# Performance work log

Hardware: AMD Instinct MI355X
Metric: run time of the kernel (lower is better)

## Reference

```python
import jax, jax.numpy as jnp
import numpy as np

N_NODES = 50000
N_EDGES = 600000
D_IN = 128
D_H = 128


def _sage_layer(h, src, dst, deg_inv, W_self, W_neigh, b):
    # gather src features along edges, sum into dst, then mean-normalize
    msum = jax.ops.segment_sum(h[src], dst, num_segments=N_NODES)  # [N, d]
    h_neigh = msum * deg_inv[:, None]
    return h @ W_self + h_neigh @ W_neigh + b


def setup_inputs() -> dict:
    key = jax.random.key(0)
    ks = jax.random.split(key, 10)
    inp = {
        'g_features': jax.random.normal(ks[0], (N_NODES, D_IN), dtype=jnp.float32),
        'src': jax.random.randint(ks[1], (N_EDGES,), 0, N_NODES, dtype=jnp.int32),
        'dst': jax.random.randint(ks[2], (N_EDGES,), 0, N_NODES, dtype=jnp.int32),
    }
    scale_in = 1.0 / np.sqrt(D_IN)
    scale_h = 1.0 / np.sqrt(D_H)
    inp['W_self1'] = jax.random.normal(ks[3], (D_IN, D_H), dtype=jnp.float32) * scale_in
    inp['W_neigh1'] = jax.random.normal(ks[4], (D_IN, D_H), dtype=jnp.float32) * scale_in
    inp['b1'] = jnp.zeros((D_H,), dtype=jnp.float32)
    inp['W_self2'] = jax.random.normal(ks[5], (D_H, D_H), dtype=jnp.float32) * scale_h
    inp['W_neigh2'] = jax.random.normal(ks[6], (D_H, D_H), dtype=jnp.float32) * scale_h
    inp['b2'] = jnp.zeros((D_H,), dtype=jnp.float32)
    inp['W_self3'] = jax.random.normal(ks[7], (D_H, D_H), dtype=jnp.float32) * scale_h
    inp['W_neigh3'] = jax.random.normal(ks[8], (D_H, D_H), dtype=jnp.float32) * scale_h
    inp['b3'] = jnp.zeros((D_H,), dtype=jnp.float32)
    return inp


def reference(g_features, src, dst, W_self1, W_neigh1, b1, W_self2, W_neigh2, b2, W_self3, W_neigh3, b3):
    # in-degree per dst node, clamped to >= 1 (DGL SAGEConv mean)
    deg = jax.ops.segment_sum(jnp.ones_like(dst, dtype=g_features.dtype), dst, num_segments=N_NODES)
    deg_inv = 1.0 / jnp.maximum(deg, 1.0)

    h = _sage_layer(g_features, src, dst, deg_inv, W_self1, W_neigh1, b1)
    h = jax.nn.relu(h)
    h = _sage_layer(h, src, dst, deg_inv, W_self2, W_neigh2, b2)
    h = jax.nn.relu(h)
    h = _sage_layer(h, src, dst, deg_inv, W_self3, W_neigh3, b3)
    return h
```

## Files before the change

kernel.cpp:

```cpp
#include <hip/hip_runtime.h>
#include <hip/hip_bf16.h>

#define N_NODES 50000
#define N_EDGES 600000
#define D 128

typedef __bf16 bf16x8 __attribute__((ext_vector_type(8)));
typedef float f32x4 __attribute__((ext_vector_type(4)));

__device__ __forceinline__ float bits2f(unsigned int u) {
    union { unsigned int i; float f; } t; t.i = u; return t.f;
}
__device__ __forceinline__ unsigned short f2bf(float x) {
    unsigned int u = __builtin_bit_cast(unsigned int, x);
    unsigned int r = (u + 0x7fff + ((u >> 16) & 1)) >> 16;
    return (unsigned short)r;
}

__global__ void hist_kernel(const int* __restrict__ dst, int* __restrict__ deg, int n) {
    int i = blockIdx.x * blockDim.x + threadIdx.x;
    if (i < n) atomicAdd(&deg[dst[i]], 1);
}

__global__ void scan1_kernel(const int* __restrict__ deg, int* __restrict__ partial,
                             int* __restrict__ blk_sums) {
    __shared__ int ws[16];
    int i = blockIdx.x * 1024 + threadIdx.x;
    int x = (i < N_NODES) ? deg[i] : 0;
    int lane = threadIdx.x & 63, wid = threadIdx.x >> 6;
    int v = x;
    #pragma unroll
    for (int off = 1; off < 64; off <<= 1) {
        int t = __shfl_up(v, off);
        if (lane >= off) v += t;
    }
    if (lane == 63) ws[wid] = v;
    __syncthreads();
    if (threadIdx.x == 0) {
        int c = 0;
        #pragma unroll
        for (int j = 0; j < 16; ++j) { int t = ws[j]; ws[j] = c; c += t; }
        blk_sums[blockIdx.x] = c;
    }
    __syncthreads();
    if (i < N_NODES) partial[i] = v - x + ws[wid];
}

__global__ void scan2_kernel(int* __restrict__ blk_sums, int nb) {
    int lane = threadIdx.x;
    int v = (lane < nb) ? blk_sums[lane] : 0;
    int x = v;
    #pragma unroll
    for (int off = 1; off < 64; off <<= 1) {
        int t = __shfl_up(v, off);
        if (lane >= off) v += t;
    }
    if (lane < nb) blk_sums[lane] = v - x;
}

__global__ void scan3_kernel(const int* __restrict__ partial, const int* __restrict__ blk_sums,
                             const int* __restrict__ deg, int* __restrict__ row_start,
                             int* __restrict__ cursor, float* __restrict__ deg_inv) {
    int i = blockIdx.x * 256 + threadIdx.x;
    if (i < N_NODES) {
        int rs = partial[i] + blk_sums[i >> 10];
        row_start[i] = rs;
        cursor[i] = rs;
        deg_inv[i] = 1.0f / fmaxf((float)deg[i], 1.0f);
    }
    if (i == 0) row_start[N_NODES] = N_EDGES;
}

__global__ void fill_kernel(const int* __restrict__ src, const int* __restrict__ dst,
                            int* __restrict__ cursor, int* __restrict__ esrc, int n) {
    int i = blockIdx.x * blockDim.x + threadIdx.x;
    if (i < n) {
        int p = atomicAdd(&cursor[dst[i]], 1);
        esrc[p] = src[i];
    }
}

__global__ void cvt_feat_kernel(const float* __restrict__ in, unsigned short* __restrict__ out, int n4) {
    int i = blockIdx.x * blockDim.x + threadIdx.x;
    if (i < n4) {
        float4 v = *(const float4*)(in + (size_t)i * 4);
        ushort4 o;
        o.x = f2bf(v.x); o.y = f2bf(v.y); o.z = f2bf(v.z); o.w = f2bf(v.w);
        *(ushort4*)(out + (size_t)i * 4) = o;
    }
}

__global__ void cvt_w_kernel(const float* w0, const float* w1, const float* w2,
                             const float* w3, const float* w4, const float* w5,
                             unsigned short* __restrict__ o) {
    int m = blockIdx.x >> 6;
    int j = (blockIdx.x & 63) * 256 + threadIdx.x;
    const float* src = m == 0 ? w0 : m == 1 ? w1 : m == 2 ? w2 : m == 3 ? w3 : m == 4 ? w4 : w5;
    int n = j >> 7, k = j & 127;
    o[m * 16384 + n * 128 + k] = f2bf(src[k * 128 + n]);
}

__device__ __forceinline__ void acc_add(float* a, uint4 v) {
    unsigned int w[4] = {v.x, v.y, v.z, v.w};
    #pragma unroll
    for (int j = 0; j < 4; ++j) {
        a[2*j]   += bits2f(w[j] << 16);
        a[2*j+1] += bits2f(w[j] & 0xffff0000u);
    }
}

#define AGG_TPB 256
__global__ __launch_bounds__(AGG_TPB) void agg_kernel(
        const unsigned short* __restrict__ h, const int* __restrict__ row_start,
        const int* __restrict__ esrc, const float* __restrict__ deg_inv,
        unsigned short* __restrict__ msum) {
    int node = blockIdx.x * (AGG_TPB / 16) + (threadIdx.x >> 4);
    if (node >= N_NODES) return;
    int l = threadIdx.x & 15;
    int s = row_start[node], e = row_start[node + 1];
    const unsigned short* hl = h + l * 8;
    float acc[8] = {0, 0, 0, 0, 0, 0, 0, 0};
    int k = s;
    for (; k + 4 <= e; k += 4) {
        int i0 = esrc[k], i1 = esrc[k + 1], i2 = esrc[k + 2], i3 = esrc[k + 3];
        uint4 v0 = *(const uint4*)(hl + (size_t)i0 * D);
        uint4 v1 = *(const uint4*)(hl + (size_t)i1 * D);
        uint4 v2 = *(const uint4*)(hl + (size_t)i2 * D);
        uint4 v3 = *(const uint4*)(hl + (size_t)i3 * D);
        acc_add(acc, v0); acc_add(acc, v1); acc_add(acc, v2); acc_add(acc, v3);
    }
    for (; k < e; ++k) {
        uint4 v = *(const uint4*)(hl + (size_t)esrc[k] * D);
        acc_add(acc, v);
    }
    float di = deg_inv[node];
    unsigned short o[8];
    #pragma unroll
    for (int j = 0; j < 8; ++j) o[j] = f2bf(acc[j] * di);
    *(uint4*)(msum + (size_t)node * D + l * 8) = *(uint4*)o;
}

__global__ __launch_bounds__(256) void gemm_kernel(
        const unsigned short* __restrict__ h, const unsigned short* __restrict__ msum,
        const unsigned short* __restrict__ WsT, const unsigned short* __restrict__ WnT,
        const float* __restrict__ bias, void* __restrict__ outp,
        int do_relu, int store_f32) {
    __shared__ char lds[49152];
    char* As = lds;
    char* Bs = lds + 16384;
    int tid = threadIdx.x;
    int l = tid & 63;
    int w = tid >> 6;
    int row0 = blockIdx.x * 64;

    f32x4 acc[4][2];
    #pragma unroll
    for (int mt = 0; mt < 4; ++mt)
        #pragma unroll
        for (int nt = 0; nt < 2; ++nt)
            acc[mt][nt] = (f32x4)0.0f;

    for (int phase = 0; phase < 2; ++phase) {
        const unsigned short* A = phase ? msum : h;
        const unsigned short* B = phase ? WnT : WsT;
        if (phase) __syncthreads();
        #pragma unroll
        for (int i = 0; i < 4; ++i) {
            int c = tid + i * 256;
            int r = c >> 4, kb = (c & 15) << 4;
            int gr = row0 + r; if (gr >= N_NODES) gr = N_NODES - 1;
            uint4 v = *(const uint4*)(A + (size_t)gr * D + ((c & 15) << 3));
            *(uint4*)(As + r * 256 + (kb ^ ((r & 7) << 4))) = v;
        }
        #pragma unroll
        for (int i = 0; i < 8; ++i) {
            int c = tid + i * 256;
            int r = c >> 4, kb = (c & 15) << 4;
            uint4 v = *(const uint4*)(B + (size_t)r * D + ((c & 15) << 3));
            *(uint4*)(Bs + r * 256 + (kb ^ ((r & 7) << 4))) = v;
        }
        __syncthreads();

        #pragma unroll
        for (int ks = 0; ks < 4; ++ks) {
            int kb = ks * 64 + ((l >> 4) << 4);
            bf16x8 a[4], b[2];
            #pragma unroll
            for (int mt = 0; mt < 4; ++mt) {
                int r = mt * 16 + (l & 15);
                a[mt] = *(const bf16x8*)(As + r * 256 + (kb ^ ((r & 7) << 4)));
            }
            #pragma unroll
            for (int nt = 0; nt < 2; ++nt) {
                int r = w * 32 + nt * 16 + (l & 15);
                b[nt] = *(const bf16x8*)(Bs + r * 256 + (kb ^ ((r & 7) << 4)));
            }
            #pragma unroll
            for (int mt = 0; mt < 4; ++mt)
                #pragma unroll
                for (int nt = 0; nt < 2; ++nt)
                    acc[mt][nt] = __builtin_amdgcn_mfma_f32_16x16x32_bf16(a[mt], b[nt], acc[mt][nt], 0, 0, 0);
        }
    }

    #pragma unroll
    for (int nt = 0; nt < 2; ++nt) {
        int col = w * 32 + nt * 16 + (l & 15);
        float bv = bias[col];
        #pragma unroll
        for (int mt = 0; mt < 4; ++mt) {
            #pragma unroll
            for (int r = 0; r < 4; ++r) {
                int grow = row0 + mt * 16 + ((l >> 4) << 2) + r;
                if (grow < N_NODES) {
                    float v = acc[mt][nt][r] + bv;
                    if (do_relu) v = fmaxf(v, 0.f);
                    if (store_f32) ((float*)outp)[(size_t)grow * D + col] = v;
                    else ((unsigned short*)outp)[(size_t)grow * D + col] = f2bf(v);
                }
            }
        }
    }
}

static inline size_t align_up(size_t x, size_t a) { return (x + a - 1) & ~(a - 1); }

extern "C" void kernel_launch(void* const* d_in, const int* in_sizes, int n_in,
                              void* d_out, int out_size, void* d_ws, size_t ws_size,
                              hipStream_t stream) {
    const float* g_feat = (const float*)d_in[0];
    const int* src = (const int*)d_in[1];
    const int* dst = (const int*)d_in[2];
    const float* Ws1 = (const float*)d_in[3];
    const float* Wn1 = (const float*)d_in[4];
    const float* b1  = (const float*)d_in[5];
    const float* Ws2 = (const float*)d_in[6];
    const float* Wn2 = (const float*)d_in[7];
    const float* b2  = (const float*)d_in[8];
    const float* Ws3 = (const float*)d_in[9];
    const float* Wn3 = (const float*)d_in[10];
    const float* b3  = (const float*)d_in[11];
    float* out = (float*)d_out;

    char* ws = (char*)d_ws;
    int* deg        = (int*)ws;            ws += align_up(N_NODES * 4, 256);
    int* row_start  = (int*)ws;            ws += align_up((N_NODES + 1) * 4, 256);
    int* cursor     = (int*)ws;            ws += align_up(N_NODES * 4, 256);
    float* deg_inv  = (float*)ws;          ws += align_up(N_NODES * 4, 256);
    int* partial    = (int*)ws;            ws += align_up(N_NODES * 4, 256);
    int* blk_sums   = (int*)ws;            ws += align_up(64 * 4, 256);
    int* esrc       = (int*)ws;            ws += align_up(N_EDGES * 4, 256);
    unsigned short* g_bf = (unsigned short*)ws;  ws += align_up((size_t)N_NODES * D * 2, 256);
    unsigned short* WT   = (unsigned short*)ws;  ws += align_up(6 * 128 * 128 * 2, 256);
    unsigned short* bufA = (unsigned short*)ws;  ws += align_up((size_t)N_NODES * D * 2, 256);
    unsigned short* bufB = (unsigned short*)ws;  ws += align_up((size_t)N_NODES * D * 2, 256);
    unsigned short* bufM = (unsigned short*)ws;  ws += align_up((size_t)N_NODES * D * 2, 256);

    hipMemsetAsync(deg, 0, N_NODES * 4, stream);
    hist_kernel<<<(N_EDGES + 255) / 256, 256, 0, stream>>>(dst, deg, N_EDGES);
    cvt_feat_kernel<<<((N_NODES * D / 4) + 255) / 256, 256, 0, stream>>>(g_feat, g_bf, N_NODES * D / 4);
    cvt_w_kernel<<<6 * 64, 256, 0, stream>>>(Ws1, Wn1, Ws2, Wn2, Ws3, Wn3, WT);
    int nb = (N_NODES + 1023) / 1024;
    scan1_kernel<<<nb, 1024, 0, stream>>>(deg, partial, blk_sums);
    scan2_kernel<<<1, 64, 0, stream>>>(blk_sums, nb);
    scan3_kernel<<<(N_NODES + 255) / 256, 256, 0, stream>>>(partial, blk_sums, deg, row_start, cursor, deg_inv);
    fill_kernel<<<(N_EDGES + 255) / 256, 256, 0, stream>>>(src, dst, cursor, esrc, N_EDGES);

    dim3 agg_grid((N_NODES * 16 + AGG_TPB - 1) / AGG_TPB);
    dim3 gemm_grid((N_NODES + 63) / 64);
    const unsigned short *WsT1 = WT, *WnT1 = WT + 16384, *WsT2 = WT + 2*16384,
                         *WnT2 = WT + 3*16384, *WsT3 = WT + 4*16384, *WnT3 = WT + 5*16384;

    agg_kernel<<<agg_grid, AGG_TPB, 0, stream>>>(g_bf, row_start, esrc, deg_inv, bufM);
    gemm_kernel<<<gemm_grid, 256, 0, stream>>>(g_bf, bufM, WsT1, WnT1, b1, bufA, 1, 0);
    agg_kernel<<<agg_grid, AGG_TPB, 0, stream>>>(bufA, row_start, esrc, deg_inv, bufM);
    gemm_kernel<<<gemm_grid, 256, 0, stream>>>(bufA, bufM, WsT2, WnT2, b2, bufB, 1, 0);
    agg_kernel<<<agg_grid, AGG_TPB, 0, stream>>>(bufB, row_start, esrc, deg_inv, bufM);
    gemm_kernel<<<gemm_grid, 256, 0, stream>>>(bufB, bufM, WsT3, WnT3, b3, out, 0, 1);
}
```

Baseline: 292.2 us.

## Fuse neighbor aggregation into layer GEMM and merge prep kernels

Fuses each layer's mean-aggregation into the GEMM kernel: every block aggregates 32 nodes directly into LDS and then runs the self and neighbor matmuls, with weight fragments held in registers. This removes the msum buffer write and read plus three launches. The feature conversion, degree histogram and weight transpose are also merged into one prep kernel to cut launch overhead. The trade-off is smaller GEMM tiles with more register pressure, and a gather-heavy phase that stalls before the MFMA phase within each block.

Result: slower. 320.6 us (+9.7%).

```diff
diff --git a/kernel.cpp b/kernel.cpp
--- a/kernel.cpp
+++ b/kernel.cpp
@@ -4,6 +4,7 @@
 #define N_NODES 50000
 #define N_EDGES 600000
 #define D 128
+#define BM 32
 
 typedef __bf16 bf16x8 __attribute__((ext_vector_type(8)));
 typedef float f32x4 __attribute__((ext_vector_type(4)));
@@ -17,9 +18,34 @@
     return (unsigned short)r;
 }
 
-__global__ void hist_kernel(const int* __restrict__ dst, int* __restrict__ deg, int n) {
-    int i = blockIdx.x * blockDim.x + threadIdx.x;
-    if (i < n) atomicAdd(&deg[dst[i]], 1);
+#define PREP_CVT_BLOCKS 6250
+#define PREP_HIST_BLOCKS 2344
+#define PREP_W_BLOCKS 384
+__global__ void prep_kernel(const float* __restrict__ feat, unsigned short* __restrict__ g_bf,
+                            const int* __restrict__ dst, int* __restrict__ deg,
+                            const float* w0, const float* w1, const float* w2,
+                            const float* w3, const float* w4, const float* w5,
+                            unsigned short* __restrict__ WT) {
+    int b = blockIdx.x;
+    if (b < PREP_CVT_BLOCKS) {
+        int i = b * 256 + threadIdx.x;
+        if (i < N_NODES * D / 4) {
+            float4 v = *(const float4*)(feat + (size_t)i * 4);
+            ushort4 o;
+            o.x = f2bf(v.x); o.y = f2bf(v.y); o.z = f2bf(v.z); o.w = f2bf(v.w);
+            *(ushort4*)(g_bf + (size_t)i * 4) = o;
+        }
+    } else if (b < PREP_CVT_BLOCKS + PREP_HIST_BLOCKS) {
+        int i = (b - PREP_CVT_BLOCKS) * 256 + threadIdx.x;
+        if (i < N_EDGES) atomicAdd(&deg[dst[i]], 1);
+    } else {
+        int j = (b - PREP_CVT_BLOCKS - PREP_HIST_BLOCKS) * 256 + threadIdx.x;
+        int m = j >> 14;
+        int e = j & 16383;
+        const float* src = m == 0 ? w0 : m == 1 ? w1 : m == 2 ? w2 : m == 3 ? w3 : m == 4 ? w4 : w5;
+        int n = e >> 7, k = e & 127;
+        WT[m * 16384 + n * 128 + k] = f2bf(src[k * 128 + n]);
+    }
 }
 
 __global__ void scan1_kernel(const int* __restrict__ deg, int* __restrict__ partial,
@@ -80,26 +106,6 @@
     }
 }
 
-__global__ void cvt_feat_kernel(const float* __restrict__ in, unsigned short* __restrict__ out, int n4) {
-    int i = blockIdx.x * blockDim.x + threadIdx.x;
-    if (i < n4) {
-        float4 v = *(const float4*)(in + (size_t)i * 4);
-        ushort4 o;
-        o.x = f2bf(v.x); o.y = f2bf(v.y); o.z = f2bf(v.z); o.w = f2bf(v.w);
-        *(ushort4*)(out + (size_t)i * 4) = o;
-    }
-}
-
-__global__ void cvt_w_kernel(const float* w0, const float* w1, const float* w2,
-                             const float* w3, const float* w4, const float* w5,
-                             unsigned short* __restrict__ o) {
-    int m = blockIdx.x >> 6;
-    int j = (blockIdx.x & 63) * 256 + threadIdx.x;
-    const float* src = m == 0 ? w0 : m == 1 ? w1 : m == 2 ? w2 : m == 3 ? w3 : m == 4 ? w4 : w5;
-    int n = j >> 7, k = j & 127;
-    o[m * 16384 + n * 128 + k] = f2bf(src[k * 128 + n]);
-}
-
 __device__ __forceinline__ void acc_add(float* a, uint4 v) {
     unsigned int w[4] = {v.x, v.y, v.z, v.w};
     #pragma unroll
@@ -109,97 +115,100 @@
     }
 }
 
-#define AGG_TPB 256
-__global__ __launch_bounds__(AGG_TPB) void agg_kernel(
+__global__ __launch_bounds__(256) void layer_kernel(
         const unsigned short* __restrict__ h, const int* __restrict__ row_start,
         const int* __restrict__ esrc, const float* __restrict__ deg_inv,
-        unsigned short* __restrict__ msum) {
-    int node = blockIdx.x * (AGG_TPB / 16) + (threadIdx.x >> 4);
-    if (node >= N_NODES) return;
-    int l = threadIdx.x & 15;
-    int s = row_start[node], e = row_start[node + 1];
-    const unsigned short* hl = h + l * 8;
-    float acc[8] = {0, 0, 0, 0, 0, 0, 0, 0};
-    int k = s;
-    for (; k + 4 <= e; k += 4) {
-        int i0 = esrc[k], i1 = esrc[k + 1], i2 = esrc[k + 2], i3 = esrc[k + 3];
-        uint4 v0 = *(const uint4*)(hl + (size_t)i0 * D);
-        uint4 v1 = *(const uint4*)(hl + (size_t)i1 * D);
-        uint4 v2 = *(const uint4*)(hl + (size_t)i2 * D);
-        uint4 v3 = *(const uint4*)(hl + (size_t)i3 * D);
-        acc_add(acc, v0); acc_add(acc, v1); acc_add(acc, v2); acc_add(acc, v3);
-    }
-    for (; k < e; ++k) {
-        uint4 v = *(const uint4*)(hl + (size_t)esrc[k] * D);
-        acc_add(acc, v);
-    }
-    float di = deg_inv[node];
-    unsigned short o[8];
-    #pragma unroll
-    for (int j = 0; j < 8; ++j) o[j] = f2bf(acc[j] * di);
-    *(uint4*)(msum + (size_t)node * D + l * 8) = *(uint4*)o;
-}
-
-__global__ __launch_bounds__(256) void gemm_kernel(
-        const unsigned short* __restrict__ h, const unsigned short* __restrict__ msum,
         const unsigned short* __restrict__ WsT, const unsigned short* __restrict__ WnT,
         const float* __restrict__ bias, void* __restrict__ outp,
         int do_relu, int store_f32) {
-    __shared__ char lds[49152];
-    char* As = lds;
-    char* Bs = lds + 16384;
+    __shared__ char lds[BM * 256 * 2];
+    char* Ah = lds;
+    char* Am = lds + BM * 256;
     int tid = threadIdx.x;
-    int l = tid & 63;
-    int w = tid >> 6;
-    int row0 = blockIdx.x * 64;
-
-    f32x4 acc[4][2];
-    #pragma unroll
-    for (int mt = 0; mt < 4; ++mt)
+    int l = tid & 63, w = tid >> 6;
+    int row0 = blockIdx.x * BM;
+
+    bf16x8 bfrag[2][2][4];
+    {
+        size_t off = (size_t)(w * 32 + (l & 15)) * D + ((l >> 4) * 8);
+        const unsigned short* Wp0 = WsT + off;
+        const unsigned short* Wp1 = WnT + off;
+        #pragma unroll
+        for (int nt = 0; nt < 2; ++nt)
+            #pragma unroll
+            for (int ks = 0; ks < 4; ++ks) {
+                bfrag[0][nt][ks] = *(const bf16x8*)(Wp0 + nt * 16 * D + ks * 32);
+                bfrag[1][nt][ks] = *(const bf16x8*)(Wp1 + nt * 16 * D + ks * 32);
+            }
+    }
+
+    #pragma unroll
+    for (int i = 0; i < 2; ++i) {
+        int c = tid + i * 256;
+        int r = c >> 4, ch = c & 15;
+        int gr = row0 + r; if (gr >= N_NODES) gr = N_NODES - 1;
+        uint4 v = *(const uint4*)(h + (size_t)gr * D + ch * 8);
+        *(uint4*)(Ah + r * 256 + ((ch << 4) ^ ((r & 7) << 4))) = v;
+    }
+
+    {
+        int gi = tid >> 4, l16 = tid & 15;
+        const unsigned short* hl = h + l16 * 8;
+        #pragma unroll
+        for (int nn = 0; nn < 2; ++nn) {
+            int r = gi * 2 + nn;
+            int node = row0 + r;
+            float acc[8] = {0, 0, 0, 0, 0, 0, 0, 0};
+            float di = 0.f;
+            if (node < N_NODES) {
+                int s = row_start[node], e = row_start[node + 1];
+                int k = s;
+                for (; k + 4 <= e; k += 4) {
+                    int i0 = esrc[k], i1 = esrc[k + 1], i2 = esrc[k + 2], i3 = esrc[k + 3];
+                    uint4 v0 = *(const uint4*)(hl + (size_t)i0 * D);
+                    uint4 v1 = *(const uint4*)(hl + (size_t)i1 * D);
+                    uint4 v2 = *(const uint4*)(hl + (size_t)i2 * D);
+                    uint4 v3 = *(const uint4*)(hl + (size_t)i3 * D);
+                    acc_add(acc, v0); acc_add(acc, v1); acc_add(acc, v2); acc_add(acc, v3);
+                }
+                for (; k < e; ++k) {
+                    uint4 v = *(const uint4*)(hl + (size_t)esrc[k] * D);
+                    acc_add(acc, v);
+                }
+                di = deg_inv[node];
+            }
+            unsigned short o[8];
+            #pragma unroll
+            for (int j = 0; j < 8; ++j) o[j] = f2bf(acc[j] * di);
+            *(uint4*)(Am + r * 256 + ((l16 << 4) ^ ((r & 7) << 4))) = *(uint4*)o;
+        }
+    }
+    __syncthreads();
+
+    f32x4 acc[2][2];
+    #pragma unroll
+    for (int mt = 0; mt < 2; ++mt)
         #pragma unroll
         for (int nt = 0; nt < 2; ++nt)
             acc[mt][nt] = (f32x4)0.0f;
 
-    for (int phase = 0; phase < 2; ++phase) {
-        const unsigned short* A = phase ? msum : h;
-        const unsigned short* B = phase ? WnT : WsT;
-        if (phase) __syncthreads();
-        #pragma unroll
-        for (int i = 0; i < 4; ++i) {
-            int c = tid + i * 256;
-            int r = c >> 4, kb = (c & 15) << 4;
-            int gr = row0 + r; if (gr >= N_NODES) gr = N_NODES - 1;
-            uint4 v = *(const uint4*)(A + (size_t)gr * D + ((c & 15) << 3));
-            *(uint4*)(As + r * 256 + (kb ^ ((r & 7) << 4))) = v;
-        }
-        #pragma unroll
-        for (int i = 0; i < 8; ++i) {
-            int c = tid + i * 256;
-            int r = c >> 4, kb = (c & 15) << 4;
-            uint4 v = *(const uint4*)(B + (size_t)r * D + ((c & 15) << 3));
-            *(uint4*)(Bs + r * 256 + (kb ^ ((r & 7) << 4))) = v;
-        }
-        __syncthreads();
-
+    #pragma unroll
+    for (int ph = 0; ph < 2; ++ph) {
+        char* Ab = ph ? Am : Ah;
         #pragma unroll
         for (int ks = 0; ks < 4; ++ks) {
             int kb = ks * 64 + ((l >> 4) << 4);
-            bf16x8 a[4], b[2];
-            #pragma unroll
-            for (int mt = 0; mt < 4; ++mt) {
+            bf16x8 a[2];
+            #pragma unroll
+            for (int mt = 0; mt < 2; ++mt) {
                 int r = mt * 16 + (l & 15);
-                a[mt] = *(const bf16x8*)(As + r * 256 + (kb ^ ((r & 7) << 4)));
-            }
-            #pragma unroll
-            for (int nt = 0; nt < 2; ++nt) {
-                int r = w * 32 + nt * 16 + (l & 15);
-                b[nt] = *(const bf16x8*)(Bs + r * 256 + (kb ^ ((r & 7) << 4)));
-            }
-            #pragma unroll
-            for (int mt = 0; mt < 4; ++mt)
+                a[mt] = *(const bf16x8*)(Ab + r * 256 + (kb ^ ((r & 7) << 4)));
+            }
+            #pragma unroll
+            for (int mt = 0; mt < 2; ++mt)
                 #pragma unroll
                 for (int nt = 0; nt < 2; ++nt)
-                    acc[mt][nt] = __builtin_amdgcn_mfma_f32_16x16x32_bf16(a[mt], b[nt], acc[mt][nt], 0, 0, 0);
+                    acc[mt][nt] = __builtin_amdgcn_mfma_f32_16x16x32_bf16(a[mt], bfrag[ph][nt][ks], acc[mt][nt], 0, 0, 0);
         }
     }
 
@@ -208,7 +217,7 @@
         int col = w * 32 + nt * 16 + (l & 15);
         float bv = bias[col];
         #pragma unroll
-        for (int mt = 0; mt < 4; ++mt) {
+        for (int mt = 0; mt < 2; ++mt) {
             #pragma unroll
             for (int r = 0; r < 4; ++r) {
                 int grow = row0 + mt * 16 + ((l >> 4) << 2) + r;
@@ -254,27 +263,21 @@
     unsigned short* WT   = (unsigned short*)ws;  ws += align_up(6 * 128 * 128 * 2, 256);
     unsigned short* bufA = (unsigned short*)ws;  ws += align_up((size_t)N_NODES * D * 2, 256);
     unsigned short* bufB = (unsigned short*)ws;  ws += align_up((size_t)N_NODES * D * 2, 256);
-    unsigned short* bufM = (unsigned short*)ws;  ws += align_up((size_t)N_NODES * D * 2, 256);
 
     hipMemsetAsync(deg, 0, N_NODES * 4, stream);
-    hist_kernel<<<(N_EDGES + 255) / 256, 256, 0, stream>>>(dst, deg, N_EDGES);
-    cvt_feat_kernel<<<((N_NODES * D / 4) + 255) / 256, 256, 0, stream>>>(g_feat, g_bf, N_NODES * D / 4);
-    cvt_w_kernel<<<6 * 64, 256, 0, stream>>>(Ws1, Wn1, Ws2, Wn2, Ws3, Wn3, WT);
+    prep_kernel<<<PREP_CVT_BLOCKS + PREP_HIST_BLOCKS + PREP_W_BLOCKS, 256, 0, stream>>>(
+        g_feat, g_bf, dst, deg, Ws1, Wn1, Ws2, Wn2, Ws3, Wn3, WT);
     int nb = (N_NODES + 1023) / 1024;
     scan1_kernel<<<nb, 1024, 0, stream>>>(deg, partial, blk_sums);
     scan2_kernel<<<1, 64, 0, stream>>>(blk_sums, nb);
     scan3_kernel<<<(N_NODES + 255) / 256, 256, 0, stream>>>(partial, blk_sums, deg, row_start, cursor, deg_inv);
     fill_kernel<<<(N_EDGES + 255) / 256, 256, 0, stream>>>(src, dst, cursor, esrc, N_EDGES);
 
-    dim3 agg_grid((N_NODES * 16 + AGG_TPB - 1) / AGG_TPB);
-    dim3 gemm_grid((N_NODES + 63) / 64);
+    dim3 grid((N_NODES + BM - 1) / BM);
     const unsigned short *WsT1 = WT, *WnT1 = WT + 16384, *WsT2 = WT + 2*16384,
                          *WnT2 = WT + 3*16384, *WsT3 = WT + 4*16384, *WnT3 = WT + 5*16384;
 
-    agg_kernel<<<agg_grid, AGG_TPB, 0, stream>>>(g_bf, row_start, esrc, deg_inv, bufM);
-    gemm_kernel<<<gemm_grid, 256, 0, stream>>>(g_bf, bufM, WsT1, WnT1, b1, bufA, 1, 0);
-    agg_kernel<<<agg_grid, AGG_TPB, 0, stream>>>(bufA, row_start, esrc, deg_inv, bufM);
-    gemm_kernel<<<gemm_grid, 256, 0, stream>>>(bufA, bufM, WsT2, WnT2, b2, bufB, 1, 0);
-    agg_kernel<<<agg_grid, AGG_TPB, 0, stream>>>(bufB, row_start, esrc, deg_inv, bufM);
-    gemm_kernel<<<gemm_grid, 256, 0, stream>>>(bufB, bufM, WsT3, WnT3, b3, out, 0, 1);
-}
+    layer_kernel<<<grid, 256, 0, stream>>>(g_bf, row_start, esrc, deg_inv, WsT1, WnT1, b1, bufA, 1, 0);
+    layer_kernel<<<grid, 256, 0, stream>>>(bufA, row_start, esrc, deg_inv, WsT2, WnT2, b2, bufB, 1, 0);
+    layer_kernel<<<grid, 256, 0, stream>>>(bufB, row_start, esrc, deg_inv, WsT3, WnT3, b3, out, 0, 1);
+}
```
